# Optimization experiments

Hardware: AMD Instinct MI355X
Metric: run time of the kernel (lower is better)

## Reference

```python
import jax, jax.numpy as jnp
import numpy as np

B, S, T = 512, 1024, 50


def setup_inputs() -> dict:
    key = jax.random.key(0)
    k1, k2, k3, k4, k5, k6, k7 = jax.random.split(key, 7)
    token_scores = jax.random.normal(k1, (B, S, T), dtype=jnp.float32)
    tags = jax.random.randint(k2, (B, S), 0, T, dtype=jnp.int64)
    # left-contiguous mask: each sequence has a random valid length >= 1
    lengths = jax.random.randint(k3, (B,), 1, S + 1)
    token_mask = (jnp.arange(S)[None, :] < lengths[:, None]).astype(jnp.int32)
    transitions = jax.random.normal(k4, (T, T), dtype=jnp.float32) * 0.1
    start_transitions = jax.random.normal(k5, (T,), dtype=jnp.float32) * 0.1
    end_transitions = jax.random.normal(k6, (T,), dtype=jnp.float32) * 0.1
    return {
        "token_scores": token_scores,
        "tags": tags,
        "token_mask": token_mask,
        "transitions": transitions,
        "start_transitions": start_transitions,
        "end_transitions": end_transitions,
    }


def _crf_log_likelihood(token_scores, tags, token_mask, transitions,
                        start_transitions, end_transitions):
    # token_scores: [B,S,T], tags: [B,S] int, token_mask: [B,S] {0,1}
    maskf = token_mask.astype(token_scores.dtype)
    maskb = token_mask.astype(bool)

    # ---- numerator: score of the gold tag path ----
    emit = jnp.take_along_axis(token_scores, tags[..., None], axis=2)[..., 0]  # [B,S]
    emit_sum = jnp.sum(emit * maskf, axis=1)
    trans_sum = jnp.sum(transitions[tags[:, :-1], tags[:, 1:]] * maskf[:, 1:], axis=1)
    start_score = start_transitions[tags[:, 0]]
    last_idx = jnp.sum(token_mask, axis=1).astype(jnp.int32) - 1          # [B]
    last_tags = jnp.take_along_axis(tags, last_idx[:, None], axis=1)[:, 0]
    end_score = end_transitions[last_tags]
    numerator = start_score + emit_sum + trans_sum + end_score            # [B]

    # ---- denominator: log partition via forward algorithm (scan over time) ----
    alpha0 = start_transitions[None, :] + token_scores[:, 0]              # [B,T]
    logits_rest = jnp.swapaxes(token_scores[:, 1:], 0, 1)                 # [S-1,B,T]
    mask_rest = jnp.swapaxes(maskb[:, 1:], 0, 1)                          # [S-1,B]

    def step(alpha, xs):
        logit_t, m_t = xs                                                 # [B,T], [B]
        # inner[b, i, j] = alpha[b,i] + transitions[i,j] + logit_t[b,j]
        inner = alpha[:, :, None] + transitions[None, :, :] + logit_t[:, None, :]
        new_alpha = jax.nn.logsumexp(inner, axis=1)                       # [B,T]
        alpha = jnp.where(m_t[:, None], new_alpha, alpha)
        return alpha, None

    alpha, _ = jax.lax.scan(step, alpha0, (logits_rest, mask_rest))
    denominator = jax.nn.logsumexp(alpha + end_transitions[None, :], axis=1)  # [B]

    return jnp.sum(numerator - denominator)  # scalar, summed over batch


def reference(token_scores, tags, token_mask, transitions,
              start_transitions, end_transitions):
    batch_size = token_scores.shape[0]
    ll = _crf_log_likelihood(token_scores, tags, token_mask, transitions,
                             start_transitions, end_transitions)
    return -ll / float(batch_size)
```

## Files before the change

kernel.cpp:

```cpp
#include <hip/hip_runtime.h>
#include <math.h>

#define CB 512
#define CS 1024
#define CT 50
#define PF 4

typedef float v2f __attribute__((ext_vector_type(2)));

__global__ void zero_out_kernel(float* out) { out[0] = 0.0f; }

__device__ __forceinline__ void wave_fence() {
    __builtin_amdgcn_wave_barrier();
    asm volatile("" ::: "memory");
}

__device__ __forceinline__ int lane0_bits(float v) {
    return __builtin_amdgcn_readlane(__float_as_int(v), 0);
}

template <int CTRL>
__device__ __forceinline__ float qperm(float v) {
    return __int_as_float(__builtin_amdgcn_update_dpp(
        0, __float_as_int(v), CTRL, 0xf, 0xf, false));
}

__global__ __launch_bounds__(128, 1) void crf_scan_kernel(
    const float* __restrict__ scores,
    const int*   __restrict__ tags,
    const int*   __restrict__ mask,
    const float* __restrict__ trans,
    const float* __restrict__ start_tr,
    const float* __restrict__ end_tr,
    float* __restrict__ out)
{
    const int b    = blockIdx.x;
    const int tid  = threadIdx.x;
    const int w    = tid >> 6;
    const int lane = tid & 63;
    const int xl   = (lane < CT) ? lane : 0;
    const int g    = lane & 3;
    const int m    = lane >> 2;
    const bool selb0 = (lane & 1) != 0;
    const bool selb1 = (lane & 2) != 0;

    __shared__ __attribute__((aligned(16))) float sTrans[CT * CT];
    __shared__ __attribute__((aligned(16))) float sP2[2][64];
    __shared__ __attribute__((aligned(16))) float sA[64];
    __shared__ __attribute__((aligned(16))) float sB[64];
    __shared__ float sLZ[2], sN[2];

    for (int k = tid; k < CT * CT; k += 128) sTrans[k] = trans[k];
    __syncthreads();

    v2f EC0[16], EC1[16];
    {
        const int i0 = 16 * g, s0 = 4 * m;
        #pragma unroll
        for (int k = 0; k < 16; ++k) {
            const int i = i0 + k;
            float e[4] = {0.f, 0.f, 0.f, 0.f};
            if (i < CT) {
                #pragma unroll
                for (int c = 0; c < 4; ++c) {
                    const int s = s0 + c;
                    if (s < CT)
                        e[c] = __expf(w == 0 ? sTrans[i * CT + s]
                                             : sTrans[s * CT + i]);
                }
            }
            EC0[k] = (v2f){e[0], e[1]};
            EC1[k] = (v2f){e[2], e[3]};
        }
    }

    const int* mrow = mask + (size_t)b * CS;
    int len = 0;
    for (int t = lane; t < CS; t += 64) len += mrow[t];
    #pragma unroll
    for (int off = 32; off; off >>= 1) len += __shfl_xor(len, off);

    const float* srow = scores + (size_t)b * CS * CT;
    const float* sx   = srow + xl;

    const int tm    = (len - 1) >> 1;
    const int count = (w == 0) ? tm : ((len >= 2) ? (len - 2 - tm) : 0);
    const int base  = (w == 0) ? 1 : (len - 2);
    const int dir   = (w == 0) ? 1 : -1;

    float st;
    if (w == 0) {
        st = (lane < CT) ? __expf(start_tr[lane] + sx[0]) : 0.f;
    } else {
        st = (lane < CT)
            ? ((len >= 2) ? __expf(end_tr[lane] + sx[(size_t)(len - 1) * CT])
                          : __expf(end_tr[lane]))
            : 0.f;
    }
    int kexp = 0;
    float* sP = sP2[w];
    const float* sPq = sP + 16 * g;

    #define STEP(EX)                                                        \
    {                                                                       \
        sP[lane] = st;                                                      \
        wave_fence();                                                       \
        const float4 p0 = *(const float4*)&sPq[0];                          \
        const float4 p1 = *(const float4*)&sPq[4];                          \
        const float4 p2 = *(const float4*)&sPq[8];                          \
        const float4 p3 = *(const float4*)&sPq[12];                         \
        wave_fence();    \
        float pv[16] = {p0.x,p0.y,p0.z,p0.w, p1.x,p1.y,p1.z,p1.w,           \
                        p2.x,p2.y,p2.z,p2.w, p3.x,p3.y,p3.z,p3.w};          \
        v2f a0 = {0.f,0.f}, a1 = {0.f,0.f};                                 \
        _Pragma("unroll")                                                   \
        for (int kk = 0; kk < 16; ++kk) {                                   \
            const v2f t2 = {pv[kk], pv[kk]};                                \
            a0 = __builtin_elementwise_fma(t2, EC0[kk], a0);                \
            a1 = __builtin_elementwise_fma(t2, EC1[kk], a1);                \
        }                                                                   \
        a0.x += qperm<0xB1>(a0.x); a0.y += qperm<0xB1>(a0.y);               \
        a1.x += qperm<0xB1>(a1.x); a1.y += qperm<0xB1>(a1.y);               \
        a0.x += qperm<0x4E>(a0.x); a0.y += qperm<0x4E>(a0.y);               \
        a1.x += qperm<0x4E>(a1.x); a1.y += qperm<0x4E>(a1.y);               \
        const float o01 = selb0 ? a0.y : a0.x;                              \
        const float o23 = selb0 ? a1.y : a1.x;                              \
        st = (selb1 ? o23 : o01) * (EX);                                    \
    }

    #define RENORM()                                                        \
    {                                                                       \
        int sb = lane0_bits(st);                                            \
        int e  = (sb >> 23) & 0xff;                                         \
        kexp  += e - 127;                                                   \
        st    *= __int_as_float((254 - e) << 23);                           \
    }

    float xpf[PF];
    #pragma unroll
    for (int k = 0; k < PF; ++k) {
        int idx = base + dir * k;
        if (idx < 0) idx = 0;
        xpf[k] = sx[(size_t)idx * CT];
    }
    int k = 0;
    while (k + PF <= count) {
        float exk[PF];
        #pragma unroll
        for (int j = 0; j < PF; ++j) exk[j] = __expf(xpf[j]);
        #pragma unroll
        for (int j = 0; j < PF; ++j) {
            int idx = base + dir * (k + PF + j);
            if (idx < 0) idx = 0;
            xpf[j] = sx[(size_t)idx * CT];
        }
        RENORM();
        STEP(exk[0]); STEP(exk[1]); STEP(exk[2]); STEP(exk[3]);
        k += PF;
    }
    for (int r = 0; k < count; ++k, ++r) {
        float e = __expf(xpf[r]);
        RENORM();
        STEP(e);
    }
    if (w == 1 && len >= 2) { RENORM(); STEP(1.0f); }
    RENORM();
    #undef STEP
    #undef RENORM

    if (w == 0) sA[lane] = (lane < CT) ? st : 0.0f;
    else        sB[lane] = (lane < CT) ? st : 0.0f;
    if (lane == 0) sLZ[w] = (float)kexp * 0.6931471805599453f;
    __syncthreads();

    const int* trow = tags + (size_t)b * CS;
    float nsum = 0.0f;
    for (int t = tid; t < CS; t += 128) {
        if (t < len) {
            int tg = trow[t];
            nsum += srow[(size_t)t * CT + tg];
            if (t >= 1) nsum += sTrans[trow[t - 1] * CT + tg];
        }
    }
    #pragma unroll
    for (int off = 32; off; off >>= 1) nsum += __shfl_xor(nsum, off);
    if (lane == 0) sN[w] = nsum;

    float den = 0.0f;
    if (w == 0) {
        float vp = sA[lane] * sB[lane];
        #pragma unroll
        for (int off = 32; off; off >>= 1) vp += __shfl_xor(vp, off);
        den = sLZ[0] + sLZ[1] + __logf(vp);
    }
    __syncthreads();

    if (tid == 0) {
        float num = sN[0] + sN[1] + start_tr[trow[0]] + end_tr[trow[len - 1]];
        atomicAdd(out, (den - num) * (1.0f / CB));
    }
}

extern "C" void kernel_launch(void* const* d_in, const int* in_sizes, int n_in,
                              void* d_out, int out_size, void* d_ws, size_t ws_size,
                              hipStream_t stream) {
    const float* scores   = (const float*)d_in[0];
    const int*   tags     = (const int*)d_in[1];
    const int*   mask     = (const int*)d_in[2];
    const float* trans    = (const float*)d_in[3];
    const float* start_tr = (const float*)d_in[4];
    const float* end_tr   = (const float*)d_in[5];
    float* out = (float*)d_out;

    zero_out_kernel<<<1, 1, 0, stream>>>(out);
    crf_scan_kernel<<<CB, 128, 0, stream>>>(scores, tags, mask, trans,
                                            start_tr, end_tr, out);
}
```

Before: 261.5 us.

## Replace LDS state broadcast with permlane swaps and DPP moves in CRF scan

Each serial recurrence step no longer writes the state vector to shared memory and reads it back as float4. It now spreads the state across lanes with permlane32/permlane16 swaps and DPP quad permutes, falling back to bpermute/swizzle when those builtins are missing. The transition-matrix register layout is remapped to fit this exchange pattern. The final reduction uses DPP row rotates by 4 and 8 instead of quad permutes. The multiply-adds are split into two accumulator chains for more ILP. The goal is to cut LDS latency and wave barriers from the latency-bound time loop, at the cost of more cross-lane instructions and a trickier index mapping.

```diff
diff --git a/kernel.cpp b/kernel.cpp
--- a/kernel.cpp
+++ b/kernel.cpp
@@ -8,21 +8,52 @@
 
 typedef float v2f __attribute__((ext_vector_type(2)));
 
+#if __has_builtin(__builtin_amdgcn_permlane16_swap)
+#define HAVE_PL16 1
+#else
+#define HAVE_PL16 0
+#endif
+#if __has_builtin(__builtin_amdgcn_permlane32_swap)
+#define HAVE_PL32 1
+#else
+#define HAVE_PL32 0
+#endif
+
 __global__ void zero_out_kernel(float* out) { out[0] = 0.0f; }
-
-__device__ __forceinline__ void wave_fence() {
-    __builtin_amdgcn_wave_barrier();
-    asm volatile("" ::: "memory");
-}
 
 __device__ __forceinline__ int lane0_bits(float v) {
     return __builtin_amdgcn_readlane(__float_as_int(v), 0);
 }
 
 template <int CTRL>
-__device__ __forceinline__ float qperm(float v) {
+__device__ __forceinline__ float dppmov(float v) {
     return __int_as_float(__builtin_amdgcn_update_dpp(
         0, __float_as_int(v), CTRL, 0xf, 0xf, false));
+}
+
+__device__ __forceinline__ void expand32(float &a, float &b, int lane) {
+#if HAVE_PL32
+    (void)lane;
+    auto r = __builtin_amdgcn_permlane32_swap(__float_as_uint(a), __float_as_uint(a),
+                                              false, false);
+    a = __uint_as_float(r[0]);
+    b = __uint_as_float(r[1]);
+#else
+    b = __int_as_float(__builtin_amdgcn_ds_bpermute((lane ^ 32) << 2,
+                                                    __float_as_int(a)));
+#endif
+}
+
+__device__ __forceinline__ void expand16(float &a, float &b, int lane) {
+    (void)lane;
+#if HAVE_PL16
+    auto r = __builtin_amdgcn_permlane16_swap(__float_as_uint(a), __float_as_uint(a),
+                                              false, false);
+    a = __uint_as_float(r[0]);
+    b = __uint_as_float(r[1]);
+#else
+    b = __int_as_float(__builtin_amdgcn_ds_swizzle(__float_as_int(a), 0x401F));
+#endif
 }
 
 __global__ __launch_bounds__(128, 1) void crf_scan_kernel(
@@ -39,39 +70,39 @@
     const int w    = tid >> 6;
     const int lane = tid & 63;
     const int xl   = (lane < CT) ? lane : 0;
-    const int g    = lane & 3;
-    const int m    = lane >> 2;
-    const bool selb0 = (lane & 1) != 0;
-    const bool selb1 = (lane & 2) != 0;
+    const bool sel4 = (lane & 4) != 0;
+    const bool sel8 = (lane & 8) != 0;
 
     __shared__ __attribute__((aligned(16))) float sTrans[CT * CT];
-    __shared__ __attribute__((aligned(16))) float sP2[2][64];
-    __shared__ __attribute__((aligned(16))) float sA[64];
-    __shared__ __attribute__((aligned(16))) float sB[64];
+    __shared__ float sA[64];
+    __shared__ float sB[64];
     __shared__ float sLZ[2], sN[2];
 
     for (int k = tid; k < CT * CT; k += 128) sTrans[k] = trans[k];
     __syncthreads();
 
+    const int F16   = HAVE_PL16 ? (lane & 16) : 0;
+    const int F32   = HAVE_PL32 ? (lane & 32) : 0;
+    const int sbase = 16 * (lane >> 4) + (lane & 3);
+
     v2f EC0[16], EC1[16];
-    {
-        const int i0 = 16 * g, s0 = 4 * m;
-        #pragma unroll
-        for (int k = 0; k < 16; ++k) {
-            const int i = i0 + k;
-            float e[4] = {0.f, 0.f, 0.f, 0.f};
-            if (i < CT) {
-                #pragma unroll
-                for (int c = 0; c < 4; ++c) {
-                    const int s = s0 + c;
-                    if (s < CT)
-                        e[c] = __expf(w == 0 ? sTrans[i * CT + s]
-                                             : sTrans[s * CT + i]);
-                }
-            }
-            EC0[k] = (v2f){e[0], e[1]};
-            EC1[k] = (v2f){e[2], e[3]};
+    #pragma unroll
+    for (int k = 0; k < 16; ++k) {
+        const int i = lane
+            ^ ((k & 1) ? (32 ^ F32) : F32)
+            ^ ((k & 2) ? (16 ^ F16) : F16)
+            ^ ((k & 4) ? 1 : 0)
+            ^ ((k & 8) ? 2 : 0);
+        float e[4];
+        #pragma unroll
+        for (int u = 0; u < 4; ++u) {
+            const int s = sbase + 4 * u;
+            e[u] = (i < CT && s < CT)
+                 ? __expf(w == 0 ? sTrans[i * CT + s] : sTrans[s * CT + i])
+                 : 0.f;
         }
+        EC0[k] = (v2f){e[0], e[1]};
+        EC1[k] = (v2f){e[2], e[3]};
     }
 
     const int* mrow = mask + (size_t)b * CS;
@@ -98,34 +129,47 @@
             : 0.f;
     }
     int kexp = 0;
-    float* sP = sP2[w];
-    const float* sPq = sP + 16 * g;
+
+    #define MAC(k, gk, suf)                                                 \
+    {                                                                       \
+        const v2f t2 = {gk, gk};                                            \
+        a0##suf = __builtin_elementwise_fma(t2, EC0[k], a0##suf);           \
+        a1##suf = __builtin_elementwise_fma(t2, EC1[k], a1##suf);           \
+    }
 
     #define STEP(EX)                                                        \
     {                                                                       \
-        sP[lane] = st;                                                      \
-        wave_fence();                                                       \
-        const float4 p0 = *(const float4*)&sPq[0];                          \
-        const float4 p1 = *(const float4*)&sPq[4];                          \
-        const float4 p2 = *(const float4*)&sPq[8];                          \
-        const float4 p3 = *(const float4*)&sPq[12];                         \
-        wave_fence();    \
-        float pv[16] = {p0.x,p0.y,p0.z,p0.w, p1.x,p1.y,p1.z,p1.w,           \
-                        p2.x,p2.y,p2.z,p2.w, p3.x,p3.y,p3.z,p3.w};          \
-        v2f a0 = {0.f,0.f}, a1 = {0.f,0.f};                                 \
-        _Pragma("unroll")                                                   \
-        for (int kk = 0; kk < 16; ++kk) {                                   \
-            const v2f t2 = {pv[kk], pv[kk]};                                \
-            a0 = __builtin_elementwise_fma(t2, EC0[kk], a0);                \
-            a1 = __builtin_elementwise_fma(t2, EC1[kk], a1);                \
-        }                                                                   \
-        a0.x += qperm<0xB1>(a0.x); a0.y += qperm<0xB1>(a0.y);               \
-        a1.x += qperm<0xB1>(a1.x); a1.y += qperm<0xB1>(a1.y);               \
-        a0.x += qperm<0x4E>(a0.x); a0.y += qperm<0x4E>(a0.y);               \
-        a1.x += qperm<0x4E>(a1.x); a1.y += qperm<0x4E>(a1.y);               \
-        const float o01 = selb0 ? a0.y : a0.x;                              \
-        const float o23 = selb0 ? a1.y : a1.x;                              \
-        st = (selb1 ? o23 : o01) * (EX);                                    \
+        float g0 = st, g1, g2, g3;                                          \
+        expand32(g0, g1, lane);                                             \
+        expand16(g0, g2, lane);                                             \
+        expand16(g1, g3, lane);                                             \
+        const float g4  = dppmov<0xB1>(g0);                                 \
+        const float g5  = dppmov<0xB1>(g1);                                 \
+        const float g6  = dppmov<0xB1>(g2);                                 \
+        const float g7  = dppmov<0xB1>(g3);                                 \
+        const float g8  = dppmov<0x4E>(g0);                                 \
+        const float g9  = dppmov<0x4E>(g1);                                 \
+        const float g10 = dppmov<0x4E>(g2);                                 \
+        const float g11 = dppmov<0x4E>(g3);                                 \
+        const float g12 = dppmov<0x4E>(g4);                                 \
+        const float g13 = dppmov<0x4E>(g5);                                 \
+        const float g14 = dppmov<0x4E>(g6);                                 \
+        const float g15 = dppmov<0x4E>(g7);                                 \
+        v2f a0lo = {0.f, 0.f}, a1lo = {0.f, 0.f};                           \
+        v2f a0hi = {0.f, 0.f}, a1hi = {0.f, 0.f};                           \
+        MAC(0,  g0,  lo) MAC(1,  g1,  lo) MAC(2,  g2,  lo) MAC(3,  g3,  lo) \
+        MAC(4,  g4,  lo) MAC(5,  g5,  lo) MAC(6,  g6,  lo) MAC(7,  g7,  lo) \
+        MAC(8,  g8,  hi) MAC(9,  g9,  hi) MAC(10, g10, hi) MAC(11, g11, hi) \
+        MAC(12, g12, hi) MAC(13, g13, hi) MAC(14, g14, hi) MAC(15, g15, hi) \
+        v2f a0 = a0lo + a0hi;                                               \
+        v2f a1 = a1lo + a1hi;                                               \
+        a0.x += dppmov<0x124>(a0.x); a0.y += dppmov<0x124>(a0.y);           \
+        a1.x += dppmov<0x124>(a1.x); a1.y += dppmov<0x124>(a1.y);           \
+        a0.x += dppmov<0x128>(a0.x); a0.y += dppmov<0x128>(a0.y);           \
+        a1.x += dppmov<0x128>(a1.x); a1.y += dppmov<0x128>(a1.y);           \
+        const float o01 = sel4 ? a0.y : a0.x;                               \
+        const float o23 = sel4 ? a1.y : a1.x;                               \
+        st = (sel8 ? o23 : o01) * (EX);                                     \
     }
 
     #define RENORM()                                                        \
@@ -166,6 +210,7 @@
     if (w == 1 && len >= 2) { RENORM(); STEP(1.0f); }
     RENORM();
     #undef STEP
+    #undef MAC
     #undef RENORM
 
     if (w == 0) sA[lane] = (lane < CT) ? st : 0.0f;
```

Measured after the change: 305.8 us. 1.17x slower.

## Double-buffer LDS exchange, split FMA chains, renormalize every step with folded scale

Applied to the files above, without the earlier changes.

The per-step LDS exchange now alternates between two shared buffers, which lets the fence-separated write and read of consecutive steps avoid reusing the same slot. The 16-long serial FMA chain is split into four independent partial accumulators to shorten the dependency latency on the critical recurrence. Renormalization now runs every step: the scale factor from the previous step's exponent is folded into the emission multiplier instead of a separate multiply per group of four steps. The final RENORM is dropped, so st leaves the loop unnormalized while kexp covers only the scales applied, which should stay consistent.

```diff
diff --git a/kernel.cpp b/kernel.cpp
--- a/kernel.cpp
+++ b/kernel.cpp
@@ -45,7 +45,7 @@
     const bool selb1 = (lane & 2) != 0;
 
     __shared__ __attribute__((aligned(16))) float sTrans[CT * CT];
-    __shared__ __attribute__((aligned(16))) float sP2[2][64];
+    __shared__ __attribute__((aligned(16))) float sP2[2][2][64];
     __shared__ __attribute__((aligned(16))) float sA[64];
     __shared__ __attribute__((aligned(16))) float sB[64];
     __shared__ float sLZ[2], sN[2];
@@ -97,43 +97,59 @@
                           : __expf(end_tr[lane]))
             : 0.f;
     }
-    int kexp = 0;
-    float* sP = sP2[w];
-    const float* sPq = sP + 16 * g;
-
-    #define STEP(EX)                                                        \
+    int kexp  = 0;
+    int e_obs = (lane0_bits(st) >> 23) & 0xff;
+
+    float*        wbuf0 = &sP2[w][0][lane];
+    float*        wbuf1 = &sP2[w][1][lane];
+    const float4* rbuf0 = (const float4*)&sP2[w][0][16 * g];
+    const float4* rbuf1 = (const float4*)&sP2[w][1][16 * g];
+
+    #define T2(V) ((v2f){(V), (V)})
+    #define MACF(A0, A1, V, K)                                              \
+        A0 = __builtin_elementwise_fma(T2(V), EC0[K], A0);                  \
+        A1 = __builtin_elementwise_fma(T2(V), EC1[K], A1);
+
+    #define STEP(WPTR, RPTR, EXS)                                           \
     {                                                                       \
-        sP[lane] = st;                                                      \
+        *(WPTR) = st;                                                       \
         wave_fence();                                                       \
-        const float4 p0 = *(const float4*)&sPq[0];                          \
-        const float4 p1 = *(const float4*)&sPq[4];                          \
-        const float4 p2 = *(const float4*)&sPq[8];                          \
-        const float4 p3 = *(const float4*)&sPq[12];                         \
+        const float4 p0 = (RPTR)[0];                                        \
+        const float4 p1 = (RPTR)[1];                                        \
+        const float4 p2 = (RPTR)[2];                                        \
+        const float4 p3 = (RPTR)[3];                                        \
         wave_fence();    \
-        float pv[16] = {p0.x,p0.y,p0.z,p0.w, p1.x,p1.y,p1.z,p1.w,           \
-                        p2.x,p2.y,p2.z,p2.w, p3.x,p3.y,p3.z,p3.w};          \
-        v2f a0 = {0.f,0.f}, a1 = {0.f,0.f};                                 \
-        _Pragma("unroll")                                                   \
-        for (int kk = 0; kk < 16; ++kk) {                                   \
-            const v2f t2 = {pv[kk], pv[kk]};                                \
-            a0 = __builtin_elementwise_fma(t2, EC0[kk], a0);                \
-            a1 = __builtin_elementwise_fma(t2, EC1[kk], a1);                \
-        }                                                                   \
+        v2f A00 = T2(p0.x) * EC0[0],  A10 = T2(p0.x) * EC1[0];              \
+        v2f A01 = T2(p1.x) * EC0[4],  A11 = T2(p1.x) * EC1[4];              \
+        v2f A02 = T2(p2.x) * EC0[8],  A12 = T2(p2.x) * EC1[8];              \
+        v2f A03 = T2(p3.x) * EC0[12], A13 = T2(p3.x) * EC1[12];             \
+        MACF(A00, A10, p0.y, 1)  MACF(A00, A10, p0.z, 2)                    \
+        MACF(A00, A10, p0.w, 3)                                             \
+        MACF(A01, A11, p1.y, 5)  MACF(A01, A11, p1.z, 6)                    \
+        MACF(A01, A11, p1.w, 7)                                             \
+        MACF(A02, A12, p2.y, 9)  MACF(A02, A12, p2.z, 10)                   \
+        MACF(A02, A12, p2.w, 11)                                            \
+        MACF(A03, A13, p3.y, 13) MACF(A03, A13, p3.z, 14)                   \
+        MACF(A03, A13, p3.w, 15)                                            \
+        v2f a0 = (A00 + A01) + (A02 + A03);                                 \
+        v2f a1 = (A10 + A11) + (A12 + A13);                                 \
         a0.x += qperm<0xB1>(a0.x); a0.y += qperm<0xB1>(a0.y);               \
         a1.x += qperm<0xB1>(a1.x); a1.y += qperm<0xB1>(a1.y);               \
         a0.x += qperm<0x4E>(a0.x); a0.y += qperm<0x4E>(a0.y);               \
         a1.x += qperm<0x4E>(a1.x); a1.y += qperm<0x4E>(a1.y);               \
+        a0 = a0 * T2(EXS);                                                  \
+        a1 = a1 * T2(EXS);                                                  \
         const float o01 = selb0 ? a0.y : a0.x;                              \
         const float o23 = selb0 ? a1.y : a1.x;                              \
-        st = (selb1 ? o23 : o01) * (EX);                                    \
-    }
-
-    #define RENORM()                                                        \
+        st = selb1 ? o23 : o01;                                             \
+    }
+
+    #define SSTEP(WPTR, RPTR, EX)                                           \
     {                                                                       \
-        int sb = lane0_bits(st);                                            \
-        int e  = (sb >> 23) & 0xff;                                         \
-        kexp  += e - 127;                                                   \
-        st    *= __int_as_float((254 - e) << 23);                           \
+        const float sc_ = __int_as_float((254 - e_obs) << 23);              \
+        kexp += e_obs - 127;                                                \
+        STEP(WPTR, RPTR, (EX) * sc_);                                       \
+        e_obs = (lane0_bits(st) >> 23) & 0xff;                              \
     }
 
     float xpf[PF];
@@ -154,19 +170,26 @@
             if (idx < 0) idx = 0;
             xpf[j] = sx[(size_t)idx * CT];
         }
-        RENORM();
-        STEP(exk[0]); STEP(exk[1]); STEP(exk[2]); STEP(exk[3]);
+        SSTEP(wbuf0, rbuf0, exk[0]);
+        SSTEP(wbuf1, rbuf1, exk[1]);
+        SSTEP(wbuf0, rbuf0, exk[2]);
+        SSTEP(wbuf1, rbuf1, exk[3]);
         k += PF;
     }
-    for (int r = 0; k < count; ++k, ++r) {
-        float e = __expf(xpf[r]);
-        RENORM();
-        STEP(e);
-    }
-    if (w == 1 && len >= 2) { RENORM(); STEP(1.0f); }
-    RENORM();
+    {
+        const int rem = count - k;
+        if (rem >= 1) { float e = __expf(xpf[0]); SSTEP(wbuf0, rbuf0, e); }
+        if (rem >= 2) { float e = __expf(xpf[1]); SSTEP(wbuf1, rbuf1, e); }
+        if (rem >= 3) { float e = __expf(xpf[2]); SSTEP(wbuf0, rbuf0, e); }
+        if (w == 1 && len >= 2) {
+            if (rem & 1) { SSTEP(wbuf1, rbuf1, 1.0f); }
+            else         { SSTEP(wbuf0, rbuf0, 1.0f); }
+        }
+    }
     #undef STEP
-    #undef RENORM
+    #undef SSTEP
+    #undef MACF
+    #undef T2
 
     if (w == 0) sA[lane] = (lane < CT) ? st : 0.0f;
     else        sB[lane] = (lane < CT) ? st : 0.0f;
```

Measured after the change: 306.0 us. 1.17x slower.

## Replace LDS broadcast with ds_bpermute and fold renormalization into emission scale

Applied to the files above, without the earlier changes.

Each scan step now gathers the 16 needed state values with ds_bpermute from registers instead of writing the state to shared memory and reading it back as float4s under wave barriers. Renormalization no longer multiplies the state immediately; the scale factor is folded into the next step's emission multiplier, which takes a multiply off the serial dependency chain. The remainder loop is unrolled into fixed cases so xpf is indexed with constants. This trades 4 LDS reads plus a write and fences for 16 bpermute instructions per step, which may or may not be cheaper on the latency-bound recurrence.

```diff
diff --git a/kernel.cpp b/kernel.cpp
--- a/kernel.cpp
+++ b/kernel.cpp
@@ -9,11 +9,6 @@
 typedef float v2f __attribute__((ext_vector_type(2)));
 
 __global__ void zero_out_kernel(float* out) { out[0] = 0.0f; }
-
-__device__ __forceinline__ void wave_fence() {
-    __builtin_amdgcn_wave_barrier();
-    asm volatile("" ::: "memory");
-}
 
 __device__ __forceinline__ int lane0_bits(float v) {
     return __builtin_amdgcn_readlane(__float_as_int(v), 0);
@@ -45,7 +40,6 @@
     const bool selb1 = (lane & 2) != 0;
 
     __shared__ __attribute__((aligned(16))) float sTrans[CT * CT];
-    __shared__ __attribute__((aligned(16))) float sP2[2][64];
     __shared__ __attribute__((aligned(16))) float sA[64];
     __shared__ __attribute__((aligned(16))) float sB[64];
     __shared__ float sLZ[2], sN[2];
@@ -74,6 +68,10 @@
         }
     }
 
+    int bpa[16];
+    #pragma unroll
+    for (int k = 0; k < 16; ++k) bpa[k] = (16 * g + k) << 2;
+
     const int* mrow = mask + (size_t)b * CS;
     int len = 0;
     for (int t = lane; t < CS; t += 64) len += mrow[t];
@@ -97,25 +95,21 @@
                           : __expf(end_tr[lane]))
             : 0.f;
     }
-    int kexp = 0;
-    float* sP = sP2[w];
-    const float* sPq = sP + 16 * g;
+    int   kexp = 0;
+    float rsc  = 1.0f;
 
     #define STEP(EX)                                                        \
     {                                                                       \
-        sP[lane] = st;                                                      \
-        wave_fence();                                                       \
-        const float4 p0 = *(const float4*)&sPq[0];                          \
-        const float4 p1 = *(const float4*)&sPq[4];                          \
-        const float4 p2 = *(const float4*)&sPq[8];                          \
-        const float4 p3 = *(const float4*)&sPq[12];                         \
-        wave_fence();    \
-        float pv[16] = {p0.x,p0.y,p0.z,p0.w, p1.x,p1.y,p1.z,p1.w,           \
-                        p2.x,p2.y,p2.z,p2.w, p3.x,p3.y,p3.z,p3.w};          \
+        const int sti = __float_as_int(st);                                 \
+        int pi[16];                                                         \
+        _Pragma("unroll")                                                   \
+        for (int kk = 0; kk < 16; ++kk)                                     \
+            pi[kk] = __builtin_amdgcn_ds_bpermute(bpa[kk], sti);            \
         v2f a0 = {0.f,0.f}, a1 = {0.f,0.f};                                 \
         _Pragma("unroll")                                                   \
         for (int kk = 0; kk < 16; ++kk) {                                   \
-            const v2f t2 = {pv[kk], pv[kk]};                                \
+            const float pv = __int_as_float(pi[kk]);                        \
+            const v2f t2 = {pv, pv};                                        \
             a0 = __builtin_elementwise_fma(t2, EC0[kk], a0);                \
             a1 = __builtin_elementwise_fma(t2, EC1[kk], a1);                \
         }                                                                   \
@@ -133,7 +127,7 @@
         int sb = lane0_bits(st);                                            \
         int e  = (sb >> 23) & 0xff;                                         \
         kexp  += e - 127;                                                   \
-        st    *= __int_as_float((254 - e) << 23);                           \
+        rsc    = __int_as_float((254 - e) << 23);                           \
     }
 
     float xpf[PF];
@@ -155,16 +149,21 @@
             xpf[j] = sx[(size_t)idx * CT];
         }
         RENORM();
-        STEP(exk[0]); STEP(exk[1]); STEP(exk[2]); STEP(exk[3]);
+        STEP(exk[0] * rsc);
+        STEP(exk[1]);
+        STEP(exk[2]);
+        STEP(exk[3]);
         k += PF;
     }
-    for (int r = 0; k < count; ++k, ++r) {
-        float e = __expf(xpf[r]);
-        RENORM();
-        STEP(e);
-    }
-    if (w == 1 && len >= 2) { RENORM(); STEP(1.0f); }
+    {
+        const int rem = count - k;
+        if (rem >= 1) { float e = __expf(xpf[0]); RENORM(); STEP(e * rsc); }
+        if (rem >= 2) { float e = __expf(xpf[1]); RENORM(); STEP(e * rsc); }
+        if (rem >= 3) { float e = __expf(xpf[2]); RENORM(); STEP(e * rsc); }
+        if (w == 1 && len >= 2) { RENORM(); STEP(rsc); }
+    }
     RENORM();
+    st *= rsc;
     #undef STEP
     #undef RENORM
 
```

Measured after the change: 283.3 us. +8.3%, slower.
